# Kernel optimization log

Measured on AMD Instinct MI355X. Metric: run time of the kernel, lower is better.

The kernel has to match this reference:

```python
import jax, jax.numpy as jnp
import numpy as np
import math

B, T, H, NH, L = 8, 1024, 192, 2, 6
FFN, K, VOCAB, OUT, WIN = 768, 3, 256, 192, 4
KC = H // NH  # per-head channels


def _get_rel(emb, t):
    pad = max(t - (WIN + 1), 0)
    start = max(WIN + 1 - t, 0)
    p = jnp.pad(emb, ((pad, pad), (0, 0)))
    return p[start:start + 2 * t - 1]


def _rel_to_abs(x):
    # [b,h,l,2l-1] -> [b,h,l,l]
    b, h, l, _ = x.shape
    x = jnp.pad(x, ((0, 0), (0, 0), (0, 0), (0, 1)))
    xf = x.reshape(b, h, l * 2 * l)
    xf = jnp.pad(xf, ((0, 0), (0, 0), (0, l - 1)))
    return xf.reshape(b, h, l + 1, 2 * l - 1)[:, :, :l, l - 1:]


def _abs_to_rel(x):
    # [b,h,l,l] -> [b,h,l,2l-1]
    b, h, l, _ = x.shape
    x = jnp.pad(x, ((0, 0), (0, 0), (0, 0), (0, l - 1)))
    xf = x.reshape(b, h, l * (2 * l - 1))
    xf = jnp.pad(xf, ((0, 0), (0, 0), (l, 0)))
    return xf.reshape(b, h, l, 2 * l)[:, :, :, 1:]


def _ln(x, g, b):
    # channels-first LayerNorm over axis 1, x: [B,C,T]
    m = jnp.mean(x, 1, keepdims=True)
    v = jnp.var(x, 1, keepdims=True)
    return (x - m) * jax.lax.rsqrt(v + 1e-5) * g[:, None] + b[:, None]


def _conv1d(x, w, b):
    y = jax.lax.conv_general_dilated(x, w, (1,), 'SAME', dimension_numbers=('NCH', 'OIH', 'NCH'))
    return y + b[:, None]


def _attn(x, attn_mask, qw, qb, kw, kb, vw, vb, ow, ob, rel_k, rel_v):
    b, d, t = x.shape
    def proj(w, bb):
        y = jnp.einsum('oc,bct->bot', w, x) + bb[:, None]
        return y.reshape(b, NH, KC, t).transpose(0, 1, 3, 2)  # [b,h,t,kc]
    q, k, v = proj(qw, qb), proj(kw, kb), proj(vw, vb)
    qs = q / math.sqrt(KC)
    scores = jnp.einsum('bhtk,bhsk->bhts', qs, k)
    scores = scores + _rel_to_abs(jnp.einsum('bhtk,mk->bhtm', qs, _get_rel(rel_k, t)))
    scores = jnp.where(attn_mask == 0, -1e4, scores)
    p = jax.nn.softmax(scores, axis=-1)
    o = jnp.einsum('bhts,bhsk->bhtk', p, v)
    o = o + jnp.einsum('bhtm,mk->bhtk', _abs_to_rel(p), _get_rel(rel_v, t))
    o = o.transpose(0, 1, 3, 2).reshape(b, d, t)
    return jnp.einsum('oc,bct->bot', ow, o) + ob[:, None]


def setup_inputs():
    key = jax.random.key(0)
    ks = iter(jax.random.split(key, 40))
    def nrm(shape, scale):
        return jax.random.normal(next(ks), shape, jnp.float32) * scale
    w = 0.05
    inp = {
        'tokens': jax.random.randint(next(ks), (B, T), 0, VOCAB),
        'x_lengths': jax.random.randint(next(ks), (B,), T // 2, T + 1),
        'emb': nrm((VOCAB, H), H ** -0.5),
        'qw': nrm((L, H, H), w), 'qb': jnp.zeros((L, H)),
        'kw': nrm((L, H, H), w), 'kb': jnp.zeros((L, H)),
        'vw': nrm((L, H, H), w), 'vb': jnp.zeros((L, H)),
        'ow': nrm((L, H, H), w), 'ob': jnp.zeros((L, H)),
        'rel_k': nrm((L, 2 * WIN + 1, KC), KC ** -0.5),
        'rel_v': nrm((L, 2 * WIN + 1, KC), KC ** -0.5),
        'ln1_g': jnp.ones((L, H)), 'ln1_b': jnp.zeros((L, H)),
        'f1w': nrm((L, FFN, H, K), w), 'f1b': jnp.zeros((L, FFN)),
        'f2w': nrm((L, H, FFN, K), w), 'f2b': jnp.zeros((L, H)),
        'ln2_g': jnp.ones((L, H)), 'ln2_b': jnp.zeros((L, H)),
        'pw': nrm((2 * OUT, H), w), 'pb': jnp.zeros((2 * OUT,)),
        'eps': jax.random.normal(next(ks), (B, OUT, T), jnp.float32),
    }
    return inp


def reference(tokens, x_lengths, emb, qw, qb, kw, kb, vw, vb, ow, ob, rel_k, rel_v,
              ln1_g, ln1_b, f1w, f1b, f2w, f2b, ln2_g, ln2_b, pw, pb, eps):
    x = emb[tokens].transpose(0, 2, 1) * math.sqrt(H)  # [B,H,T]
    x_mask = (jnp.arange(T) < x_lengths[:, None]).astype(x.dtype)[:, None, :]  # [B,1,T]
    attn_mask = x_mask[:, :, None, :] * x_mask[:, :, :, None]  # [B,1,T,T]
    x = x * x_mask
    for i in range(L):
        y = _attn(x, attn_mask, qw[i], qb[i], kw[i], kb[i], vw[i], vb[i], ow[i], ob[i], rel_k[i], rel_v[i])
        x = _ln(x + y, ln1_g[i], ln1_b[i])
        y = jax.nn.relu(_conv1d(x * x_mask, f1w[i], f1b[i]))
        y = _conv1d(y * x_mask, f2w[i], f2b[i]) * x_mask
        x = _ln(x + y, ln2_g[i], ln2_b[i])
    x = x * x_mask
    stats = (jnp.einsum('oc,bct->bot', pw, x) + pb[:, None]) * x_mask
    m, logs = stats[:, :OUT], stats[:, OUT:]
    z = m + eps * jnp.exp(logs) * x_mask
    return (z, m, logs, x, x_mask)
```

## Files before the change

kernel.cpp:

```cpp
#include <hip/hip_runtime.h>
#include <math.h>

#define BN 8
#define TN 1024
#define HN 192
#define NHN 2
#define KCN 96
#define LN 6
#define FFNN 768
#define OUTN 192
#define QSTR 104
#define GSTR 200
#define M0S 12.0f

typedef short bfrag __attribute__((ext_vector_type(8)));
typedef float f32x4 __attribute__((ext_vector_type(4)));

__device__ __forceinline__ short f2bf(float f) {
    union { float f; unsigned u; } v; v.f = f;
    unsigned r = v.u + 0x7fffu + ((v.u >> 16) & 1u);
    return (short)(r >> 16);
}
__device__ __forceinline__ float bf2f(short s) {
    union { unsigned u; float f; } v;
    v.u = ((unsigned)(unsigned short)s) << 16;
    return v.f;
}
__device__ __forceinline__ int pack2(float a, float b) {
    return (int)(unsigned short)f2bf(a) | (((int)(unsigned short)f2bf(b)) << 16);
}

#define QSCALE 0.10206207261596575f

__global__ void k_cvtall(const float* __restrict__ qw, const float* __restrict__ kw,
        const float* __restrict__ vw, const float* __restrict__ qb,
        const float* __restrict__ kb, const float* __restrict__ vb,
        const float* __restrict__ ow, const float* __restrict__ pw,
        const float* __restrict__ f1w, const float* __restrict__ f2w,
        short* __restrict__ wqkv, float* __restrict__ bqkv,
        short* __restrict__ wo16, short* __restrict__ wp16,
        short* __restrict__ wf1, short* __restrict__ wf2) {
    const int N0 = LN * 576 * 192;
    const int N1 = LN * 576;
    const int N2 = LN * HN * HN;
    const int N3 = 2 * OUTN * HN;
    const int N4 = LN * FFNN * HN * 3;
    int i = blockIdx.x * 256 + threadIdx.x;
    if (i < N0) {
        int c = i % 192, r = (i / 192) % 576, l = i / (192 * 576);
        float val, sc = 1.f;
        if (r < 192) { val = qw[((size_t)l * 192 + r) * 192 + c]; sc = QSCALE; }
        else if (r < 384) val = kw[((size_t)l * 192 + (r - 192)) * 192 + c];
        else val = vw[((size_t)l * 192 + (r - 384)) * 192 + c];
        wqkv[i] = f2bf(val * sc);
        return;
    }
    i -= N0;
    if (i < N1) {
        int r = i % 576, l = i / 576;
        bqkv[i] = (r < 192) ? qb[l * 192 + r] * QSCALE
                : (r < 384) ? kb[l * 192 + r - 192]
                            : vb[l * 192 + r - 384];
        return;
    }
    i -= N1;
    if (i < N2) { wo16[i] = f2bf(ow[i]); return; }
    i -= N2;
    if (i < N3) { wp16[i] = f2bf(pw[i]); return; }
    i -= N3;
    if (i < N4) {
        int tap = i % 3, c = (i / 3) % HN, m = (i / (3 * HN)) % FFNN, l = i / (3 * HN * FFNN);
        wf1[(((size_t)l * 3 + tap) * FFNN + m) * HN + c] = f2bf(f1w[i]);
        return;
    }
    i -= N4;
    if (i < N4) {
        int tap = i % 3, c = (i / 3) % FFNN, m = (i / (3 * FFNN)) % HN, l = i / (3 * FFNN * HN);
        wf2[(((size_t)l * 3 + tap) * HN + m) * FFNN + c] = f2bf(f2w[i]);
    }
}

__global__ __launch_bounds__(256) void k_embed(const int* __restrict__ tok,
        const int* __restrict__ lens, const float* __restrict__ emb,
        float* __restrict__ x, short* __restrict__ xb) {
    __shared__ float s[HN][65];
    const int b = blockIdx.y, t0 = blockIdx.x * 64, tid = threadIdx.x;
    const int len = lens[b];
    for (int idx = tid; idx < 64 * HN; idx += 256) {
        int tt = idx / HN, c = idx % HN;
        int t = t0 + tt;
        float v = 0.f;
        if (t < len) v = emb[tok[b * TN + t] * HN + c] * 13.856406460551018f;
        s[c][tt] = v;
    }
    __syncthreads();
    for (int idx = tid; idx < 64 * HN; idx += 256) {
        int c = idx >> 6, tt = idx & 63;
        x[((size_t)b * HN + c) * TN + t0 + tt] = s[c][tt];
    }
    for (int idx = tid; idx < 64 * 96; idx += 256) {
        int tt = idx / 96, p = idx % 96;
        ((int*)xb)[((size_t)(b * TN + t0 + tt)) * 96 + p] = pack2(s[2 * p][tt], s[2 * p + 1][tt]);
    }
}

template <bool MERGE, bool MASK_OUT>
__global__ __launch_bounds__(256) void k_g192(
        const short* __restrict__ W, const short* __restrict__ X,
        const float* __restrict__ bias, float* __restrict__ Y,
        const short* __restrict__ accP, const float* __restrict__ lPp,
        const int* __restrict__ lens, int M) {
    __shared__ short Wt[64 * GSTR];
    __shared__ short Xt[64 * GSTR];
    __shared__ float linv[128];
    const int b = blockIdx.z, m0 = blockIdx.y * 64, t0 = blockIdx.x * 64;
    const int len = lens[b];
    const int tid = threadIdx.x;
    const int w = tid >> 6, lane = tid & 63, col = lane & 15, quad = lane >> 4;

    if (t0 >= len) {
        if (MASK_OUT) {
            const int mbase = m0 + w * 16 + quad * 4;
#pragma unroll
            for (int st = 0; st < 4; ++st) {
                int t = t0 + st * 16 + col;
#pragma unroll
                for (int reg = 0; reg < 4; ++reg)
                    Y[((size_t)b * M + mbase + reg) * TN + t] = 0.f;
            }
        }
        return;
    }

    if (MERGE) {
        if (tid < 128) {
            int tt = tid & 63, h = tid >> 6;
            float l = 0.f;
#pragma unroll
            for (int sh = 0; sh < 4; ++sh)
                l += lPp[(((size_t)sh * BN + b) * NHN + h) * TN + t0 + tt];
            linv[tid] = (l > 0.f) ? 1.f / l : 0.f;
        }
        __syncthreads();
    }
    for (int i = tid; i < 1536; i += 256) {
        int mm = i / 24, part = i % 24;
        *(int4*)(Wt + mm * GSTR + part * 8) =
            *(const int4*)(W + ((size_t)(m0 + mm)) * 192 + part * 8);
    }
    for (int i = tid; i < 1536; i += 256) {
        int tt = i / 24, part = i % 24;
        if (!MERGE) {
            *(int4*)(Xt + tt * GSTR + part * 8) =
                *(const int4*)(X + ((size_t)(b * TN + t0 + tt)) * 192 + part * 8);
        } else {
            const size_t base = ((size_t)(b * TN + t0 + tt)) * 192 + part * 8;
            const size_t HSq = (size_t)BN * TN * HN;
            float a[8];
#pragma unroll
            for (int c = 0; c < 8; ++c) a[c] = 0.f;
#pragma unroll
            for (int sh = 0; sh < 4; ++sh) {
                int4 v = *(const int4*)(accP + sh * HSq + base);
                const short* sv = (const short*)&v;
#pragma unroll
                for (int c = 0; c < 8; ++c) a[c] += bf2f(sv[c]);
            }
            float li = linv[(part >= 12 ? 64 : 0) + tt];
            int4 o;
            int* oi = (int*)&o;
#pragma unroll
            for (int c = 0; c < 4; ++c) oi[c] = pack2(a[2 * c] * li, a[2 * c + 1] * li);
            *(int4*)(Xt + tt * GSTR + part * 8) = o;
        }
    }
    __syncthreads();

    f32x4 acc[4];
#pragma unroll
    for (int st = 0; st < 4; ++st) acc[st] = (f32x4){0.f, 0.f, 0.f, 0.f};
#pragma unroll
    for (int ks = 0; ks < 6; ++ks) {
        bfrag af = *(const bfrag*)(Wt + (w * 16 + col) * GSTR + ks * 32 + quad * 8);
#pragma unroll
        for (int st = 0; st < 4; ++st) {
            bfrag bf = *(const bfrag*)(Xt + (st * 16 + col) * GSTR + ks * 32 + quad * 8);
            acc[st] = __builtin_amdgcn_mfma_f32_16x16x32_bf16(af, bf, acc[st], 0, 0, 0);
        }
    }

    const int mbase = m0 + w * 16 + quad * 4;
    float bs[4];
#pragma unroll
    for (int reg = 0; reg < 4; ++reg) bs[reg] = bias[mbase + reg];
#pragma unroll
    for (int st = 0; st < 4; ++st) {
        int t = t0 + st * 16 + col;
        bool om = MASK_OUT && (t >= len);
#pragma unroll
        for (int reg = 0; reg < 4; ++reg) {
            float u = acc[st][reg] + bs[reg];
            if (om) u = 0.f;
            Y[((size_t)b * M + mbase + reg) * TN + t] = u;
        }
    }
}

__global__ __launch_bounds__(256) void k_qkv2(
        const short* __restrict__ W, const short* __restrict__ X,
        const float* __restrict__ bias, short* __restrict__ qo,
        short* __restrict__ ko, short* __restrict__ vo,
        const int* __restrict__ lens) {
    __shared__ short Wt[64 * GSTR];
    __shared__ short Xt[64 * GSTR];
    const int b = blockIdx.z, m0 = blockIdx.y * 64, t0 = blockIdx.x * 64;
    const int len = lens[b];
    const int tid = threadIdx.x;
    const int w = tid >> 6, lane = tid & 63, col = lane & 15, quad = lane >> 4;
    const int proj = m0 / 192;
    const int mbase = m0 + w * 16 + quad * 4;
    const int mloc = mbase - proj * 192;

    if (t0 >= len) {
        if (proj == 1) return;
#pragma unroll
        for (int st = 0; st < 4; ++st) {
            int t = t0 + st * 16 + col;
            if (proj == 0) {
                int2 z = {0, 0};
                *(int2*)(qo + ((size_t)(b * TN + t)) * 192 + mloc) = z;
            } else {
#pragma unroll
                for (int reg = 0; reg < 4; ++reg)
                    vo[((size_t)b * 192 + mloc + reg) * TN + t] = 0;
            }
        }
        return;
    }

    for (int i = tid; i < 1536; i += 256) {
        int mm = i / 24, part = i % 24;
        *(int4*)(Wt + mm * GSTR + part * 8) =
            *(const int4*)(W + ((size_t)(m0 + mm)) * 192 + part * 8);
    }
    for (int i = tid; i < 1536; i += 256) {
        int tt = i / 24, part = i % 24;
        *(int4*)(Xt + tt * GSTR + part * 8) =
            *(const int4*)(X + ((size_t)(b * TN + t0 + tt)) * 192 + part * 8);
    }
    __syncthreads();

    f32x4 acc[4];
#pragma unroll
    for (int st = 0; st < 4; ++st) acc[st] = (f32x4){0.f, 0.f, 0.f, 0.f};
#pragma unroll
    for (int ks = 0; ks < 6; ++ks) {
        bfrag af = *(const bfrag*)(Wt + (w * 16 + col) * GSTR + ks * 32 + quad * 8);
#pragma unroll
        for (int st = 0; st < 4; ++st) {
            bfrag bf = *(const bfrag*)(Xt + (st * 16 + col) * GSTR + ks * 32 + quad * 8);
            acc[st] = __builtin_amdgcn_mfma_f32_16x16x32_bf16(af, bf, acc[st], 0, 0, 0);
        }
    }

    float bs[4];
#pragma unroll
    for (int reg = 0; reg < 4; ++reg) bs[reg] = bias[mbase + reg];
#pragma unroll
    for (int st = 0; st < 4; ++st) {
        int t = t0 + st * 16 + col;
        float v[4];
#pragma unroll
        for (int reg = 0; reg < 4; ++reg) v[reg] = acc[st][reg] + bs[reg];
        if (proj < 2) {
            short* dst = (proj == 0) ? qo : ko;
            int2 pk;
            pk.x = pack2(v[0], v[1]);
            pk.y = pack2(v[2], v[3]);
            *(int2*)(dst + ((size_t)(b * TN + t)) * 192 + mloc) = pk;
        } else {
#pragma unroll
            for (int reg = 0; reg < 4; ++reg)
                vo[((size_t)b * 192 + mloc + reg) * TN + t] = f2bf(v[reg]);
        }
    }
}

template <int TAPS, int TT, bool RELU, bool MASK_OUT, int OUTK, int KSPLIT>
__global__ __launch_bounds__(256) void k_mgemm(
        const short* __restrict__ W, const short* __restrict__ X,
        const float* __restrict__ bias, void* __restrict__ Yv,
        float* __restrict__ Yv2, float* __restrict__ Yv3,
        const int* __restrict__ lens, int M, int Cin) {
    constexpr int P = (TAPS - 1) / 2;
    constexpr int NST = TT / 16;
    __shared__ short Wt[TAPS][64][72];
    __shared__ short Xt[TT + 2 * P][72];

    const int b = blockIdx.z;
    const int mtiles = gridDim.y / KSPLIT;
    const int kg = blockIdx.y / mtiles;
    const int m0 = (blockIdx.y % mtiles) * 64;
    const int t0 = blockIdx.x * TT;
    const int len = lens[b];
    const int tid = threadIdx.x;
    const int w = tid >> 6;
    const int lane = tid & 63;
    const int col = lane & 15;
    const int quad = lane >> 4;
    const int mbase = m0 + w * 16 + quad * 4;

    if (MASK_OUT && t0 >= len) {
#pragma unroll
        for (int st = 0; st < NST; ++st) {
            int t = t0 + st * 16 + col;
            if (OUTK == 0) {
                float* dst = (KSPLIT > 1) ? (kg == 0 ? (float*)Yv : (kg == 1 ? Yv2 : Yv3))
                                          : (float*)Yv;
#pragma unroll
                for (int reg = 0; reg < 4; ++reg)
                    dst[((size_t)b * M + mbase + reg) * TN + t] = 0.f;
            } else {
                int2 z = {0, 0};
                *(int2*)((short*)Yv + ((size_t)(b * TN + t)) * M + mbase) = z;
            }
        }
        return;
    }

    f32x4 acc[NST];
#pragma unroll
    for (int st = 0; st < NST; ++st) acc[st] = (f32x4){0.f, 0.f, 0.f, 0.f};

    const int cspan = Cin / KSPLIT;
    const int cbeg = kg * cspan;
    const int cend = cbeg + cspan;
    for (int c0 = cbeg; c0 < cend; c0 += 64) {
        __syncthreads();
        for (int i = tid; i < TAPS * 64 * 8; i += 256) {
            int tap = i / (64 * 8);
            int mm = (i / 8) & 63;
            int part = i & 7;
            *(int4*)(&Wt[tap][mm][part * 8]) =
                *(const int4*)(W + ((size_t)tap * M + m0 + mm) * Cin + c0 + part * 8);
        }
        for (int i = tid; i < (TT + 2 * P) * 8; i += 256) {
            int tt = i >> 3;
            int part = i & 7;
            int t = t0 + tt - P;
            int4 v = {0, 0, 0, 0};
            if (t >= 0 && t < TN)
                v = *(const int4*)(X + ((size_t)b * TN + t) * Cin + c0 + part * 8);
            *(int4*)(&Xt[tt][part * 8]) = v;
        }
        __syncthreads();
#pragma unroll
        for (int ks = 0; ks < 2; ++ks) {
#pragma unroll
            for (int tap = 0; tap < TAPS; ++tap) {
                bfrag af = *(const bfrag*)(&Wt[tap][w * 16 + col][ks * 32 + quad * 8]);
#pragma unroll
                for (int st = 0; st < NST; ++st) {
                    bfrag bf = *(const bfrag*)(&Xt[st * 16 + col + tap][ks * 32 + quad * 8]);
                    acc[st] = __builtin_amdgcn_mfma_f32_16x16x32_bf16(af, bf, acc[st], 0, 0, 0);
                }
            }
        }
    }

    float bs[4];
#pragma unroll
    for (int reg = 0; reg < 4; ++reg)
        bs[reg] = (KSPLIT > 1 && kg) ? 0.f : bias[mbase + reg];
#pragma unroll
    for (int st = 0; st < NST; ++st) {
        int t = t0 + st * 16 + col;
        bool om = MASK_OUT && (t >= len);
        float v[4];
#pragma unroll
        for (int reg = 0; reg < 4; ++reg) {
            float u = acc[st][reg] + bs[reg];
            if (RELU) u = fmaxf(u, 0.f);
            if (om) u = 0.f;
            v[reg] = u;
        }
        if (OUTK == 0) {
            float* dst = (KSPLIT > 1) ? (kg == 0 ? (float*)Yv : (kg == 1 ? Yv2 : Yv3))
                                      : (float*)Yv;
#pragma unroll
            for (int reg = 0; reg < 4; ++reg)
                dst[((size_t)b * M + mbase + reg) * TN + t] = v[reg];
        } else {
            int2 pk;
            pk.x = pack2(v[0], v[1]);
            pk.y = pack2(v[2], v[3]);
            *(int2*)((short*)Yv + ((size_t)(b * TN + t)) * M + mbase) = pk;
        }
    }
}

__global__ __launch_bounds__(512, 4) void k_attn4(
        const short* __restrict__ Q, const short* __restrict__ K,
        const short* __restrict__ V, const float* __restrict__ relk,
        const float* __restrict__ relv, short* __restrict__ accP,
        float* __restrict__ lP, const int* __restrict__ lens) {
    __shared__ short kt[64 * QSTR];
    __shared__ short vt[96 * 72];
    __shared__ short Pt[128 * 72];
    __shared__ short rbt[16 * QSTR];
    __shared__ float rels[128 * 12];
    __shared__ float sband[128 * 12];
    __shared__ float rvs[9 * 96];

    const int b = blockIdx.z;
    const int h = blockIdx.y >> 2, sh = blockIdx.y & 3;
    const int t0 = blockIdx.x * 128;
    const int len = lens[b];
    const int tid = threadIdx.x;
    const int w = tid >> 6;
    const int lane = tid & 63;
    const int col = lane & 15;
    const int quad = lane >> 4;

    if (t0 >= len) {
        if (tid < 128)
            lP[(((size_t)sh * BN + b) * NHN + h) * TN + t0 + tid] = 0.f;
        return;
    }

    const short* Qb = Q + ((size_t)b * TN + t0) * HN + h * KCN;
    const short* Kb = K + ((size_t)b * TN + sh * 256) * HN + h * KCN;
    const short* Vb = V + ((size_t)b * HN + h * KCN) * TN + sh * 256;

    bfrag qf[3];
#pragma unroll
    for (int ks = 0; ks < 3; ++ks)
        qf[ks] = *(const bfrag*)(Qb + (size_t)(w * 16 + col) * HN + ks * 32 + quad * 8);

    for (int i = tid; i < 9 * 96; i += 512) rvs[i] = relv[i];
    for (int i = tid; i < 16 * 96; i += 512) {
        int r = i / 96, c = i % 96;
        rbt[r * QSTR + c] = (r < 9) ? f2bf(relk[r * 96 + c]) : (short)0;
    }
    for (int i = tid; i < 128 * 12; i += 512) sband[i] = -1e30f;
    __syncthreads();

    {
        f32x4 rc = (f32x4){0.f, 0.f, 0.f, 0.f};
#pragma unroll
        for (int ks = 0; ks < 3; ++ks) {
            bfrag bf = *(const bfrag*)(rbt + col * QSTR + ks * 32 + quad * 8);
            rc = __builtin_amdgcn_mfma_f32_16x16x32_bf16(qf[ks], bf, rc, 0, 0, 0);
        }
        if (col < 12) {
#pragma unroll
            for (int reg = 0; reg < 4; ++reg)
                rels[(w * 16 + quad * 4 + reg) * 12 + col] = rc[reg];
        }
    }

    float lsum[4];
    f32x4 accv[6];
#pragma unroll
    for (int r = 0; r < 4; ++r) lsum[r] = 0.f;
#pragma unroll
    for (int n = 0; n < 6; ++n) accv[n] = (f32x4){0.f, 0.f, 0.f, 0.f};

    const int rem = len - sh * 256;
    const int nj = (rem <= 0) ? 0 : ((rem >= 256) ? 4 : ((rem + 63) >> 6));

    for (int j = 0; j < nj; ++j) {
        const int s0g = sh * 256 + j * 64;
        __syncthreads();
        for (int i = tid; i < 768; i += 512) {
            int row = i / 12, part = i % 12;
            *(int4*)(kt + row * QSTR + part * 8) =
                *(const int4*)(Kb + ((size_t)(j * 64 + row)) * HN + part * 8);
        }
        for (int i = tid; i < 768; i += 512) {
            int c = i >> 3, part = i & 7;
            *(int4*)(vt + c * 72 + part * 8) =
                *(const int4*)(Vb + (size_t)c * TN + j * 64 + part * 8);
        }
        __syncthreads();

        f32x4 sacc[4];
#pragma unroll
        for (int st = 0; st < 4; ++st) sacc[st] = (f32x4){0.f, 0.f, 0.f, 0.f};
#pragma unroll
        for (int ks = 0; ks < 3; ++ks) {
#pragma unroll
            for (int st = 0; st < 4; ++st) {
                bfrag bf = *(const bfrag*)(kt + (st * 16 + col) * QSTR + ks * 32 + quad * 8);
                sacc[st] = __builtin_amdgcn_mfma_f32_16x16x32_bf16(qf[ks], bf, sacc[st], 0, 0, 0);
            }
        }

#pragma unroll
        for (int reg = 0; reg < 4; ++reg) {
            const int lq = w * 16 + quad * 4 + reg;
            const int qg = t0 + lq;
#pragma unroll
            for (int st = 0; st < 4; ++st) {
                int sg = s0g + st * 16 + col;
                float v = sacc[st][reg];
                int d = sg - qg + 4;
                bool inb = (d >= 0) && (d <= 8);
                if (inb) v += rels[lq * 12 + d];
                if (sg >= len) v = -1e4f;
                if (inb) sband[lq * 12 + d] = v;
                float p = __expf(v - M0S);
                lsum[reg] += p;
                Pt[lq * 72 + st * 16 + col] = f2bf(p);
            }
        }
#pragma unroll
        for (int ks = 0; ks < 2; ++ks) {
            bfrag af = *(const bfrag*)(Pt + (w * 16 + col) * 72 + ks * 32 + quad * 8);
#pragma unroll
            for (int nt = 0; nt < 6; ++nt) {
                bfrag bf = *(const bfrag*)(vt + (nt * 16 + col) * 72 + ks * 32 + quad * 8);
                accv[nt] = __builtin_amdgcn_mfma_f32_16x16x32_bf16(af, bf, accv[nt], 0, 0, 0);
            }
        }
    }

#pragma unroll
    for (int reg = 0; reg < 4; ++reg) {
        lsum[reg] += __shfl_xor(lsum[reg], 1);
        lsum[reg] += __shfl_xor(lsum[reg], 2);
        lsum[reg] += __shfl_xor(lsum[reg], 4);
        lsum[reg] += __shfl_xor(lsum[reg], 8);
    }
    __syncthreads();

    short* aout = accP + (size_t)sh * BN * TN * HN;
#pragma unroll
    for (int reg = 0; reg < 4; ++reg) {
        const int lq = w * 16 + quad * 4 + reg;
        const int qg = t0 + lq;
        float pb[9];
#pragma unroll
        for (int d = 0; d < 9; ++d)
            pb[d] = __expf(sband[lq * 12 + d] - M0S);
#pragma unroll
        for (int nt = 0; nt < 6; ++nt) {
            int c = nt * 16 + col;
            float r = accv[nt][reg];
#pragma unroll
            for (int d = 0; d < 9; ++d) r += pb[d] * rvs[d * 96 + c];
            aout[((size_t)(b * TN + qg)) * HN + h * KCN + c] = f2bf(r);
        }
        if (col == 0)
            lP[(((size_t)sh * BN + b) * NHN + h) * TN + qg] = lsum[reg];
    }
}

template <int NADD>
__global__ __launch_bounds__(256) void k_ln(float* __restrict__ x,
        const float* __restrict__ y, const float* __restrict__ y2,
        const float* __restrict__ y3, const float* __restrict__ g,
        const float* __restrict__ bb, short* __restrict__ xb,
        const int* __restrict__ lens) {
    __shared__ float s[HN][33];
    __shared__ float red1[256], red2[256];
    __shared__ float mu[32], rs[32];
    const int b = blockIdx.y;
    const int t0 = blockIdx.x * 32;
    const int tid = threadIdx.x;
    const int len = lens[b];

    if (t0 >= len) {
        for (int idx = tid; idx < 32 * 96; idx += 256)
            ((int*)xb)[((size_t)(b * TN + t0 + idx / 96)) * 96 + idx % 96] = 0;
        return;
    }

    for (int idx = tid; idx < HN * 32; idx += 256) {
        int c = idx >> 5, tt = idx & 31;
        size_t gi = ((size_t)b * HN + c) * TN + t0 + tt;
        float v = x[gi] + y[gi];
        if (NADD >= 2) v += y2[gi];
        if (NADD >= 3) v += y3[gi];
        s[c][tt] = v;
    }
    __syncthreads();
    int tt = tid & 31, grp = tid >> 5;
    float sum = 0.f, sum2 = 0.f;
    for (int c = grp * 24; c < grp * 24 + 24; ++c) {
        float v = s[c][tt];
        sum += v;
        sum2 += v * v;
    }
    red1[tid] = sum;
    red2[tid] = sum2;
    __syncthreads();
    if (tid < 32) {
        float tot = 0.f, tot2 = 0.f;
#pragma unroll
        for (int gg = 0; gg < 8; ++gg) { tot += red1[gg * 32 + tid]; tot2 += red2[gg * 32 + tid]; }
        float mean = tot / (float)HN;
        float var = tot2 / (float)HN - mean * mean;
        mu[tid] = mean;
        rs[tid] = rsqrtf(var + 1e-5f);
    }
    __syncthreads();
    for (int idx = tid; idx < HN * 32; idx += 256) {
        int c = idx >> 5, t2 = idx & 31;
        float v = (s[c][t2] - mu[t2]) * rs[t2] * g[c] + bb[c];
        x[((size_t)b * HN + c) * TN + t0 + t2] = v;
    }
    for (int idx = tid; idx < 32 * 96; idx += 256) {
        int t2 = idx / 96, p = idx % 96;
        int c0 = 2 * p;
        float v0 = (s[c0][t2] - mu[t2]) * rs[t2] * g[c0] + bb[c0];
        float v1 = (s[c0 + 1][t2] - mu[t2]) * rs[t2] * g[c0 + 1] + bb[c0 + 1];
        if (t0 + t2 >= len) { v0 = 0.f; v1 = 0.f; }
        ((int*)xb)[((size_t)(b * TN + t0 + t2)) * 96 + p] = pack2(v0, v1);
    }
}

__global__ void k_final(const float* __restrict__ stats, const float* __restrict__ x,
        const float* __restrict__ eps, const int* __restrict__ lens,
        float* __restrict__ out) {
    int idx = blockIdx.x * 256 + threadIdx.x;
    int t = idx % TN;
    int o = (idx / TN) % OUTN;
    int b = idx / (TN * OUTN);
    float maskv = (t < lens[b]) ? 1.f : 0.f;
    const size_t S = (size_t)BN * OUTN * TN;
    float m = stats[((size_t)(b * 2 * OUTN) + o) * TN + t];
    float ls = stats[((size_t)(b * 2 * OUTN) + OUTN + o) * TN + t];
    float e = eps[idx];
    out[idx] = m + e * expf(ls) * maskv;
    out[S + idx] = m;
    out[2 * S + idx] = ls;
    out[3 * S + idx] = x[idx] * maskv;
    if (o == 0) out[4 * S + (size_t)b * TN + t] = maskv;
}

extern "C" void kernel_launch(void* const* d_in, const int* in_sizes, int n_in,
                              void* d_out, int out_size, void* d_ws, size_t ws_size,
                              hipStream_t stream) {
    const int* tok = (const int*)d_in[0];
    const int* lens = (const int*)d_in[1];
    const float* emb = (const float*)d_in[2];
    const float* qw = (const float*)d_in[3];
    const float* qb = (const float*)d_in[4];
    const float* kw = (const float*)d_in[5];
    const float* kb = (const float*)d_in[6];
    const float* vw = (const float*)d_in[7];
    const float* vb = (const float*)d_in[8];
    const float* ow = (const float*)d_in[9];
    const float* ob = (const float*)d_in[10];
    const float* relk = (const float*)d_in[11];
    const float* relv = (const float*)d_in[12];
    const float* ln1g = (const float*)d_in[13];
    const float* ln1b = (const float*)d_in[14];
    const float* f1w = (const float*)d_in[15];
    const float* f1b = (const float*)d_in[16];
    const float* f2w = (const float*)d_in[17];
    const float* f2b = (const float*)d_in[18];
    const float* ln2g = (const float*)d_in[19];
    const float* ln2b = (const float*)d_in[20];
    const float* pw = (const float*)d_in[21];
    const float* pb = (const float*)d_in[22];
    const float* eps = (const float*)d_in[23];

    const size_t BHT = (size_t)BN * HN * TN;
    float* ws = (float*)d_ws;
    float* x = ws;
    float* yf = ws + BHT;
    short* s_xb = (short*)(ws + 2 * BHT);
    short* s_ln = (short*)(ws + 2 * BHT + BHT / 2);
    short* s_q  = (short*)(ws + 3 * BHT);
    short* s_k  = (short*)(ws + 3 * BHT + BHT / 2);
    short* s_v  = (short*)(ws + 4 * BHT);
    float* p1   = ws + 3 * BHT;
    float* p2   = ws + 4 * BHT;
    short* accP = (short*)(ws + 5 * BHT);
    short* s_y1 = (short*)(ws + 5 * BHT);
    float* stats = ws + 5 * BHT;
    short* wqkv = (short*)(ws + 7 * BHT);
    short* wo16 = wqkv + (size_t)LN * 3 * HN * HN;
    short* wp16 = wo16 + (size_t)LN * HN * HN;
    short* wf1_16 = wp16 + (size_t)2 * OUTN * HN;
    short* wf2_16 = wf1_16 + (size_t)LN * 3 * FFNN * HN;
    float* bqkv = (float*)(wf2_16 + (size_t)LN * 3 * FFNN * HN);
    float* lP = bqkv + (size_t)LN * 576;

    {
        long total = (long)LN * 576 * 192 + LN * 576 + LN * HN * HN + 2 * OUTN * HN
                   + 2L * LN * FFNN * HN * 3;
        k_cvtall<<<dim3((unsigned)((total + 255) / 256)), 256, 0, stream>>>(
            qw, kw, vw, qb, kb, vb, ow, pw, f1w, f2w,
            wqkv, bqkv, wo16, wp16, wf1_16, wf2_16);
    }

    dim3 gemb(TN / 64, BN);
    k_embed<<<gemb, 256, 0, stream>>>(tok, lens, emb, x, s_xb);

    dim3 gqkv(TN / 64, 9, BN);
    dim3 gattn(TN / 128, NHN * 4, BN);
    dim3 goproj(TN / 64, HN / 64, BN);
    dim3 gf1(TN / 128, FFNN / 64, BN);
    dim3 gf2(TN / 128, 9, BN);
    dim3 gln(TN / 32, BN);

    for (int i = 0; i < LN; ++i) {
        const short* qkvwi = wqkv + (size_t)i * 576 * 192;
        const float* qkvbi = bqkv + (size_t)i * 576;
        const short* owi = wo16 + (size_t)i * HN * HN;
        const short* f1wi = wf1_16 + (size_t)i * 3 * FFNN * HN;
        const short* f2wi = wf2_16 + (size_t)i * 3 * FFNN * HN;
        const float* obi = ob + (size_t)i * HN;
        const float* rki = relk + (size_t)i * 9 * KCN;
        const float* rvi = relv + (size_t)i * 9 * KCN;
        const float* l1gi = ln1g + (size_t)i * HN;
        const float* l1bi = ln1b + (size_t)i * HN;
        const float* f1bi = f1b + (size_t)i * FFNN;
        const float* f2bi = f2b + (size_t)i * HN;
        const float* l2gi = ln2g + (size_t)i * HN;
        const float* l2bi = ln2b + (size_t)i * HN;

        k_qkv2<<<gqkv, 256, 0, stream>>>(qkvwi, s_xb, qkvbi, s_q, s_k, s_v, lens);
        k_attn4<<<gattn, 512, 0, stream>>>(s_q, s_k, s_v, rki, rvi, accP, lP, lens);
        k_g192<true, false><<<goproj, 256, 0, stream>>>(owi, nullptr, obi, yf, accP, lP, lens, HN);
        k_ln<1><<<gln, 256, 0, stream>>>(x, yf, nullptr, nullptr, l1gi, l1bi, s_ln, lens);
        k_mgemm<3, 128, true, true, 1, 1><<<gf1, 256, 0, stream>>>(f1wi, s_ln, f1bi, s_y1, nullptr, nullptr, lens, FFNN, HN);
        k_mgemm<3, 128, false, true, 0, 3><<<gf2, 256, 0, stream>>>(f2wi, s_y1, f2bi, yf, p1, p2, lens, HN, FFNN);
        k_ln<3><<<gln, 256, 0, stream>>>(x, yf, p1, p2, l2gi, l2bi, s_xb, lens);
    }

    dim3 gstat(TN / 64, (2 * OUTN) / 64, BN);
    k_g192<false, true><<<gstat, 256, 0, stream>>>(wp16, s_xb, pb, stats, nullptr, nullptr, lens, 2 * OUTN);
    k_final<<<dim3((unsigned)(BHT / 256)), 256, 0, stream>>>(stats, x, eps, lens, (float*)d_out);
}
```

Baseline: 852.4 us.

## Prefetch K/V tiles into registers, cache band probs, halve LN tile

The attention kernel now issues the global loads for the next K/V tile into registers before computing on the current tile. This overlaps global memory latency with MFMA work at the cost of extra registers. It also stores the exponentiated band probabilities directly so the epilogue no longer recomputes exp, initialising the band to zero instead of -1e30. Separately, the LayerNorm kernel processes 16 timesteps per block instead of 32, doubling the block count to improve occupancy and parallelism.

Result: slower. 871.8 us (+2.3%).

```diff
diff --git a/kernel.cpp b/kernel.cpp
--- a/kernel.cpp
+++ b/kernel.cpp
@@ -442,7 +442,7 @@
         int r = i / 96, c = i % 96;
         rbt[r * QSTR + c] = (r < 9) ? f2bf(relk[r * 96 + c]) : (short)0;
     }
-    for (int i = tid; i < 128 * 12; i += 512) sband[i] = -1e30f;
+    for (int i = tid; i < 128 * 12; i += 512) sband[i] = 0.f;
     __syncthreads();
 
     {
@@ -469,20 +469,29 @@
     const int rem = len - sh * 256;
     const int nj = (rem <= 0) ? 0 : ((rem >= 256) ? 4 : ((rem + 63) >> 6));
 
+    short* dst0 = kt + (tid / 12) * QSTR + (tid % 12) * 8;
+    short* dst1 = (tid < 256) ? kt + ((tid + 512) / 12) * QSTR + ((tid + 512) % 12) * 8
+                              : vt + ((tid - 256) >> 3) * 72 + ((tid - 256) & 7) * 8;
+    short* dst2 = vt + ((tid + 256) >> 3) * 72 + ((tid + 256) & 7) * 8;
+    int4 pre0, pre1, pre2;
+#define ATTN_ISSUE(jj) do { \
+        pre0 = *(const int4*)(Kb + ((size_t)((jj) * 64 + tid / 12)) * HN + (tid % 12) * 8); \
+        pre1 = (tid < 256) \
+            ? *(const int4*)(Kb + ((size_t)((jj) * 64 + (tid + 512) / 12)) * HN + ((tid + 512) % 12) * 8) \
+            : *(const int4*)(Vb + (size_t)((tid - 256) >> 3) * TN + (jj) * 64 + ((tid - 256) & 7) * 8); \
+        pre2 = *(const int4*)(Vb + (size_t)((tid + 256) >> 3) * TN + (jj) * 64 + ((tid + 256) & 7) * 8); \
+    } while (0)
+
+    if (nj > 0) ATTN_ISSUE(0);
+
     for (int j = 0; j < nj; ++j) {
         const int s0g = sh * 256 + j * 64;
         __syncthreads();
-        for (int i = tid; i < 768; i += 512) {
-            int row = i / 12, part = i % 12;
-            *(int4*)(kt + row * QSTR + part * 8) =
-                *(const int4*)(Kb + ((size_t)(j * 64 + row)) * HN + part * 8);
-        }
-        for (int i = tid; i < 768; i += 512) {
-            int c = i >> 3, part = i & 7;
-            *(int4*)(vt + c * 72 + part * 8) =
-                *(const int4*)(Vb + (size_t)c * TN + j * 64 + part * 8);
-        }
+        *(int4*)dst0 = pre0;
+        *(int4*)dst1 = pre1;
+        *(int4*)dst2 = pre2;
         __syncthreads();
+        if (j + 1 < nj) ATTN_ISSUE(j + 1);
 
         f32x4 sacc[4];
 #pragma unroll
@@ -508,8 +517,8 @@
                 bool inb = (d >= 0) && (d <= 8);
                 if (inb) v += rels[lq * 12 + d];
                 if (sg >= len) v = -1e4f;
-                if (inb) sband[lq * 12 + d] = v;
                 float p = __expf(v - M0S);
+                if (inb) sband[lq * 12 + d] = p;
                 lsum[reg] += p;
                 Pt[lq * 72 + st * 16 + col] = f2bf(p);
             }
@@ -524,6 +533,7 @@
             }
         }
     }
+#undef ATTN_ISSUE
 
 #pragma unroll
     for (int reg = 0; reg < 4; ++reg) {
@@ -542,7 +552,7 @@
         float pb[9];
 #pragma unroll
         for (int d = 0; d < 9; ++d)
-            pb[d] = __expf(sband[lq * 12 + d] - M0S);
+            pb[d] = sband[lq * 12 + d];
 #pragma unroll
         for (int nt = 0; nt < 6; ++nt) {
             int c = nt * 16 + col;
@@ -562,22 +572,22 @@
         const float* __restrict__ y3, const float* __restrict__ g,
         const float* __restrict__ bb, short* __restrict__ xb,
         const int* __restrict__ lens) {
-    __shared__ float s[HN][33];
+    __shared__ float s[HN][17];
     __shared__ float red1[256], red2[256];
-    __shared__ float mu[32], rs[32];
+    __shared__ float mu[16], rs[16];
     const int b = blockIdx.y;
-    const int t0 = blockIdx.x * 32;
+    const int t0 = blockIdx.x * 16;
     const int tid = threadIdx.x;
     const int len = lens[b];
 
     if (t0 >= len) {
-        for (int idx = tid; idx < 32 * 96; idx += 256)
+        for (int idx = tid; idx < 16 * 96; idx += 256)
             ((int*)xb)[((size_t)(b * TN + t0 + idx / 96)) * 96 + idx % 96] = 0;
         return;
     }
 
-    for (int idx = tid; idx < HN * 32; idx += 256) {
-        int c = idx >> 5, tt = idx & 31;
+    for (int idx = tid; idx < HN * 16; idx += 256) {
+        int c = idx >> 4, tt = idx & 15;
         size_t gi = ((size_t)b * HN + c) * TN + t0 + tt;
         float v = x[gi] + y[gi];
         if (NADD >= 2) v += y2[gi];
@@ -585,9 +595,9 @@
         s[c][tt] = v;
     }
     __syncthreads();
-    int tt = tid & 31, grp = tid >> 5;
+    int tt = tid & 15, grp = tid >> 4;
     float sum = 0.f, sum2 = 0.f;
-    for (int c = grp * 24; c < grp * 24 + 24; ++c) {
+    for (int c = grp * 12; c < grp * 12 + 12; ++c) {
         float v = s[c][tt];
         sum += v;
         sum2 += v * v;
@@ -595,22 +605,22 @@
     red1[tid] = sum;
     red2[tid] = sum2;
     __syncthreads();
-    if (tid < 32) {
+    if (tid < 16) {
         float tot = 0.f, tot2 = 0.f;
 #pragma unroll
-        for (int gg = 0; gg < 8; ++gg) { tot += red1[gg * 32 + tid]; tot2 += red2[gg * 32 + tid]; }
+        for (int gg = 0; gg < 16; ++gg) { tot += red1[gg * 16 + tid]; tot2 += red2[gg * 16 + tid]; }
         float mean = tot / (float)HN;
         float var = tot2 / (float)HN - mean * mean;
         mu[tid] = mean;
         rs[tid] = rsqrtf(var + 1e-5f);
     }
     __syncthreads();
-    for (int idx = tid; idx < HN * 32; idx += 256) {
-        int c = idx >> 5, t2 = idx & 31;
+    for (int idx = tid; idx < HN * 16; idx += 256) {
+        int c = idx >> 4, t2 = idx & 15;
         float v = (s[c][t2] - mu[t2]) * rs[t2] * g[c] + bb[c];
         x[((size_t)b * HN + c) * TN + t0 + t2] = v;
     }
-    for (int idx = tid; idx < 32 * 96; idx += 256) {
+    for (int idx = tid; idx < 16 * 96; idx += 256) {
         int t2 = idx / 96, p = idx % 96;
         int c0 = 2 * p;
         float v0 = (s[c0][t2] - mu[t2]) * rs[t2] * g[c0] + bb[c0];
@@ -705,7 +715,7 @@
     dim3 goproj(TN / 64, HN / 64, BN);
     dim3 gf1(TN / 128, FFNN / 64, BN);
     dim3 gf2(TN / 128, 9, BN);
-    dim3 gln(TN / 32, BN);
+    dim3 gln(TN / 16, BN);
 
     for (int i = 0; i < LN; ++i) {
         const short* qkvwi = wqkv + (size_t)i * 576 * 192;
```
